# Kernel tuning notes

Measured on AMD Instinct MI355X. Metric: run time of the kernel, lower is better.

The kernel has to match this reference:

```python
import jax, jax.numpy as jnp
import numpy as np

B, N, F, D, TOPK, EXTRA = 32, 128, 10, 64, 20, 25
BN = B * N
EPS = 1e-5
SLOPE = 0.2  # GDN GraphLayer leaky_relu negative slope


def _cosine(a, b):
    na = jnp.maximum(jnp.linalg.norm(a, axis=-1), 1e-12)
    nb = jnp.maximum(jnp.linalg.norm(b, axis=-1), 1e-12)
    return (a @ b.T) / (na[:, None] * nb[None, :])


def _segment_softmax(logits, seg, num):
    m = jax.ops.segment_max(logits, seg, num_segments=num)
    m = jnp.where(jnp.isfinite(m), m, 0.0)  # empty segments
    e = jnp.exp(logits - m[seg])
    s = jax.ops.segment_sum(e, seg, num_segments=num)
    return e / jnp.maximum(s[seg], 1e-12)


def setup_inputs() -> dict:
    key = jax.random.key(0)
    ks = jax.random.split(key, 12)
    r = lambda i, shape, s=1.0: jax.random.normal(ks[i], shape, dtype=jnp.float32) * s
    return dict(
        data=r(0, (B, N, F)),
        emb=r(1, (N, D)) * 0.3,                       # nn.Embedding(node_num, dim)
        W1=r(2, (F, D)) * (1.0 / np.sqrt(F)),         # GraphLayer lin
        att_i1=r(3, (2 * D,)) * 0.1,                  # att on concat(h, emb)
        att_j1=r(4, (2 * D,)) * 0.1,
        bias1=jnp.zeros((D,), jnp.float32),
        bn1_g=jnp.ones((D,), jnp.float32),
        bn1_b=jnp.zeros((D,), jnp.float32),
        P=r(5, (BN, BN)) * (1.0 / np.sqrt(BN)),       # extra_pram
        W2=r(6, (D, D)) * (1.0 / np.sqrt(D)),         # GraphLayer1 lin
        att_i2=r(7, (D,)) * 0.1,
        att_j2=r(8, (D,)) * 0.1,
        bias2=jnp.zeros((D,), jnp.float32),
        bnO_g=jnp.ones((D,), jnp.float32),
        bnO_b=jnp.zeros((D,), jnp.float32),
        W_out=r(9, (D, 1)) * (1.0 / np.sqrt(D)),      # OutLayer Linear(dim,1)
        b_out=jnp.zeros((1,), jnp.float32),
        org_edge_index=jnp.zeros((2, 2), jnp.int32),  # dead arg in original forward
    )


def _forward(data, emb, W1, att_i1, att_j1, bias1, bn1_g, bn1_b, P, W2,
             att_i2, att_j2, bias2, bnO_g, bnO_b, W_out, b_out):
    x = data.reshape(BN, F)

    # ---- learned top-k graph from detached embedding cosine similarity ----
    w = jax.lax.stop_gradient(emb)              # weights_arr = detach()
    cos = _cosine(w, w)                         # [N, N]
    topv, topi = jax.lax.top_k(cos, TOPK)       # [N, TOPK]
    cos_w = jnp.tile(topv.reshape(-1), B)       # [B*N*TOPK]
    src0 = topi.reshape(-1)                     # gated_j (source)
    dst0 = jnp.repeat(jnp.arange(N), TOPK)      # gated_i (target)
    offs = jnp.repeat(jnp.arange(B) * N, N * TOPK)
    src = jnp.tile(src0, B) + offs
    dst = jnp.tile(dst0, B) + offs

    # ---- GraphLayer (GAT-style with embedding keys, edge weight = cos) ----
    all_emb = jnp.tile(emb, (B, 1))             # [BN, D]
    h = x @ W1                                  # [BN, D]
    kf = jnp.concatenate([h, all_emb], axis=-1) # [BN, 2D]
    si, sj = kf @ att_i1, kf @ att_j1           # [BN]
    score = jax.nn.leaky_relu(si[dst] + sj[src], SLOPE) * cos_w
    alpha = _segment_softmax(score, dst, BN)
    agg = jax.ops.segment_sum(h[src] * alpha[:, None], dst, num_segments=BN) + bias1
    mu, var = agg.mean(0), agg.var(0)           # BatchNorm1d (batch stats)
    gcn = jax.nn.relu(bn1_g * (agg - mu) / jnp.sqrt(var + EPS) + bn1_b)

    # ---- extra-feature branch (always taken: P is [BN, BN]) ----
    ef = P.T @ gcn                              # (gcn_out.T @ P).T
    g = jnp.concatenate([gcn, ef], axis=0)      # [2BN, D]
    cos2 = _cosine(g, g)                        # [2BN, 2BN]
    topv2, topi2 = jax.lax.top_k(cos2, EXTRA)
    corrs = topv2[:BN].reshape(-1)              # [BN*EXTRA]
    src2 = jnp.repeat(jnp.arange(BN), EXTRA)    # extra_i = edge_index[0] (source)
    dst2 = topi2[:BN].reshape(-1)               # extra_j = edge_index[1] (target)

    # ---- GraphLayer1 (no embedding keys, no BN in GNNLayer1.forward) ----
    h2 = g @ W2                                 # [2BN, D]
    s2 = jax.nn.leaky_relu((h2 @ att_i2)[dst2] + (h2 @ att_j2)[src2], SLOPE) * corrs
    alpha2 = _segment_softmax(s2, dst2, 2 * BN)
    agg2 = jax.ops.segment_sum(h2[src2] * alpha2[:, None], dst2, num_segments=2 * BN) + bias2
    gcn2 = jax.nn.relu(agg2)[:BN]

    # ---- output head: mul by embedding, BN over channels, Linear(D,1) ----
    x3 = gcn2.reshape(B, N, D) * emb[None]      # [B, N, D]
    mu2, var2 = x3.mean((0, 1)), x3.var((0, 1)) # BatchNorm1d over channel D
    x4 = jax.nn.relu(bnO_g * (x3 - mu2) / jnp.sqrt(var2 + EPS) + bnO_b)
    out = x4 @ W_out + b_out                    # [B, N, 1]; dropout = identity (eval)
    return out.reshape(-1, N)                   # [B, N]


def reference(data, emb, W1, att_i1, att_j1, bias1, bn1_g, bn1_b, P, W2,
              att_i2, att_j2, bias2, bnO_g, bnO_b, W_out, b_out, org_edge_index):
    # org_edge_index is dead in the original forward (only cached, never consumed)
    return _forward(data, emb, W1, att_i1, att_j1, bias1, bn1_g, bn1_b, P, W2,
                    att_i2, att_j2, bias2, bnO_g, bnO_b, W_out, b_out)
```

## Files before the change

kernel.cpp:

```cpp
#include <hip/hip_runtime.h>
#include <hip/hip_bf16.h>
#include <math.h>

#define DEV __device__ __forceinline__

constexpr int Bb   = 32;
constexpr int Nn   = 128;
constexpr int Ff   = 10;
constexpr int Dd   = 64;
constexpr int TOPK = 20;
constexpr int EXTRA= 25;
constexpr int BN   = 4096;
constexpr int TBN  = 8192;
constexpr int RC   = 16;
constexpr int CAND_CAP = 1024;
constexpr float EPS   = 1e-5f;
constexpr float SLOPE = 0.2f;

DEV unsigned int fenc(float f){
  unsigned int b = __float_as_uint(f);
  return (b & 0x80000000u) ? ~b : (b | 0x80000000u);
}
DEV float fdec(unsigned int u){
  unsigned int b = (u & 0x80000000u) ? (u & 0x7FFFFFFFu) : ~u;
  return __uint_as_float(b);
}

__global__ void k_zero(float* __restrict__ p, int n){
  int i = blockIdx.x*256 + threadIdx.x;
  if(i < n) p[i] = 0.f;
}

__global__ void k_emb_norm(const float* __restrict__ emb, float* __restrict__ norms){
  int i = blockIdx.x, d = threadIdx.x;
  float v = emb[i*Dd + d];
  float s = v*v;
  for(int o=32;o>0;o>>=1) s += __shfl_down(s, o, 64);
  if(d==0) norms[i] = fmaxf(sqrtf(s), 1e-12f);
}

__global__ void k_emb_topk(const float* __restrict__ emb, const float* __restrict__ norms,
                           float* __restrict__ topv, int* __restrict__ topi){
  __shared__ float se[Dd];
  __shared__ float sc[Nn];
  int i = blockIdx.x, t = threadIdx.x;
  if(t < Dd) se[t] = emb[i*Dd + t];
  __syncthreads();
  float dot = 0.f;
  for(int d=0; d<Dd; d++) dot += se[d]*emb[t*Dd + d];
  float v = dot/(norms[i]*norms[t]);
  sc[t] = v;
  __syncthreads();
  int rank = 0;
  for(int j=0; j<Nn; j++){
    float vj = sc[j];
    rank += (vj > v) || (vj == v && j < t);
  }
  if(rank < TOPK){
    topv[i*TOPK + rank] = v;
    topi[i*TOPK + rank] = t;
  }
}

__global__ void k_h1(const float* __restrict__ data, const float* __restrict__ emb,
                     const float* __restrict__ W1, const float* __restrict__ ai1,
                     const float* __restrict__ aj1,
                     float* __restrict__ h, float* __restrict__ si, float* __restrict__ sj){
  int r = blockIdx.x, d = threadIdx.x;
  int node = r & (Nn-1);
  __shared__ float xr[Ff];
  if(d < Ff) xr[d] = data[r*Ff + d];
  __syncthreads();
  float hv = 0.f;
  #pragma unroll
  for(int f=0; f<Ff; f++) hv += xr[f]*W1[f*Dd + d];
  h[r*Dd + d] = hv;
  float e = emb[node*Dd + d];
  float a = hv*ai1[d] + e*ai1[Dd + d];
  float b = hv*aj1[d] + e*aj1[Dd + d];
  for(int o=32;o>0;o>>=1){ a += __shfl_down(a,o,64); b += __shfl_down(b,o,64); }
  if(d==0){ si[r] = a; sj[r] = b; }
}

__global__ void k_agg1(const float* __restrict__ h, const float* __restrict__ si,
                       const float* __restrict__ sj, const float* __restrict__ topv,
                       const int* __restrict__ topi, const float* __restrict__ bias1,
                       float* __restrict__ agg){
  int r = blockIdx.x, d = threadIdx.x;
  int b = r >> 7, node = r & (Nn-1);
  __shared__ float sal[TOPK];
  __shared__ int   ssrc[TOPK];
  if(d < TOPK){
    int s = b*Nn + topi[node*TOPK + d];
    float sc = si[r] + sj[s];
    sc = sc >= 0.f ? sc : SLOPE*sc;
    sal[d] = sc * topv[node*TOPK + d];
    ssrc[d] = s;
  }
  __syncthreads();
  float m = -INFINITY;
  #pragma unroll
  for(int k=0;k<TOPK;k++) m = fmaxf(m, sal[k]);
  float al[TOPK]; float ssum = 0.f;
  #pragma unroll
  for(int k=0;k<TOPK;k++){ al[k] = expf(sal[k]-m); ssum += al[k]; }
  float inv = 1.0f/fmaxf(ssum, 1e-12f);
  float acc = 0.f;
  #pragma unroll
  for(int k=0;k<TOPK;k++) acc += al[k]*inv*h[ssrc[k]*Dd + d];
  agg[r*Dd + d] = acc + bias1[d];
}

__global__ void k_colstats(const float* __restrict__ x, float* __restrict__ mu, float* __restrict__ var){
  int c = blockIdx.x, t = threadIdx.x;
  float s = 0.f, s2 = 0.f;
  for(int r=t; r<BN; r+=256){ float v = x[r*Dd + c]; s += v; s2 += v*v; }
  __shared__ float ls[256], ls2[256];
  ls[t]=s; ls2[t]=s2; __syncthreads();
  for(int o=128;o>0;o>>=1){
    if(t<o){ ls[t]+=ls[t+o]; ls2[t]+=ls2[t+o]; }
    __syncthreads();
  }
  if(t==0){ float m = ls[0]/BN; mu[c]=m; var[c]=ls2[0]/BN - m*m; }
}

__global__ void k_bnrelu1(const float* __restrict__ agg, const float* __restrict__ mu,
                          const float* __restrict__ var, const float* __restrict__ gamma,
                          const float* __restrict__ beta, float* __restrict__ g){
  int idx = blockIdx.x*256 + threadIdx.x;
  int c = idx & (Dd-1);
  float v = agg[idx];
  float y = gamma[c]*(v - mu[c])/sqrtf(var[c]+EPS) + beta[c];
  g[idx] = fmaxf(y, 0.f);
}

__global__ __launch_bounds__(256) void k_ef1(const float* __restrict__ P, const float* __restrict__ gcn,
                                             float* __restrict__ part){
  __shared__ float Pt[16*128];
  __shared__ float Gt[16*64];
  int t = threadIdx.x;
  int jbase = blockIdx.x*128;
  int r0 = blockIdx.y*256;
  int row = t >> 4, col4 = (t & 15)*4;
  int tr = t >> 4, tc = t & 15;
  float acc[8][4] = {};
  for(int step=0; step<16; step++){
    int r = r0 + step*16;
    float4 pv0 = *(const float4*)&P[(size_t)(r+row)*BN + jbase + col4];
    float4 pv1 = *(const float4*)&P[(size_t)(r+row)*BN + jbase + col4 + 64];
    float4 gv  = *(const float4*)&gcn[(r+row)*Dd + col4];
    __syncthreads();
    *(float4*)&Pt[row*128 + col4]      = pv0;
    *(float4*)&Pt[row*128 + col4 + 64] = pv1;
    *(float4*)&Gt[row*64 + col4] = gv;
    __syncthreads();
    #pragma unroll
    for(int rr=0; rr<16; rr++){
      float4 pa0 = *(float4*)&Pt[rr*128 + tr*8];
      float4 pa1 = *(float4*)&Pt[rr*128 + tr*8 + 4];
      float4 gb  = *(float4*)&Gt[rr*64 + tc*4];
      float pav[8] = {pa0.x,pa0.y,pa0.z,pa0.w,pa1.x,pa1.y,pa1.z,pa1.w};
      float gbv[4] = {gb.x,gb.y,gb.z,gb.w};
      #pragma unroll
      for(int a=0;a<8;a++)
        #pragma unroll
        for(int b=0;b<4;b++) acc[a][b] += pav[a]*gbv[b];
    }
  }
  float* dst = part + ((size_t)blockIdx.y*BN + jbase)*Dd;
  #pragma unroll
  for(int a=0;a<8;a++){
    float4 v = make_float4(acc[a][0],acc[a][1],acc[a][2],acc[a][3]);
    *(float4*)&dst[(tr*8+a)*Dd + tc*4] = v;
  }
}

__global__ void k_ef2(const float* __restrict__ part, float* __restrict__ ef){
  int i = blockIdx.x*256 + threadIdx.x;
  float4 s = make_float4(0.f,0.f,0.f,0.f);
  #pragma unroll
  for(int c=0;c<RC;c++){
    float4 v = *(const float4*)&part[(size_t)c*BN*Dd + (size_t)i*4];
    s.x += v.x; s.y += v.y; s.z += v.z; s.w += v.w;
  }
  *(float4*)&ef[(size_t)i*4] = s;
}

__global__ void k_gn(const float* __restrict__ x, float* __restrict__ gn){
  int r = blockIdx.x, d = threadIdx.x;
  float v = x[(size_t)r*Dd + d];
  float s = v*v;
  for(int o=32;o>0;o>>=1) s += __shfl_down(s, o, 64);
  s = __shfl(s, 0, 64);
  float inv = 1.0f/fmaxf(sqrtf(s), 1e-12f);
  gn[(size_t)r*Dd + d] = v*inv;
}

__global__ __launch_bounds__(256) void k_sgemm(const float* __restrict__ gn,
                                               int rbase, float* __restrict__ S,
                                               float* __restrict__ Smax){
  __shared__ __align__(16) float A[64*128];
  __shared__ __align__(16) float Bs[64*128];
  int t = threadIdx.x;
  int ctile = blockIdx.x*128;
  int rtile = rbase + blockIdx.y*128;
  int q = t >> 4, m0 = t & 15;
  #pragma unroll
  for(int l=0;l<8;l++){
    int m = m0 + 16*l;
    float4 av = *(const float4*)&gn[(size_t)(rtile+m)*Dd + q*4];
    float4 bv = *(const float4*)&gn[(size_t)(ctile+m)*Dd + q*4];
    A[(q*4+0)*128 + m] = av.x; A[(q*4+1)*128 + m] = av.y;
    A[(q*4+2)*128 + m] = av.z; A[(q*4+3)*128 + m] = av.w;
    Bs[(q*4+0)*128 + m] = bv.x; Bs[(q*4+1)*128 + m] = bv.y;
    Bs[(q*4+2)*128 + m] = bv.z; Bs[(q*4+3)*128 + m] = bv.w;
  }
  __syncthreads();
  int tr = t >> 4;
  int tc = t & 15;
  float acc[8][8] = {};
  #pragma unroll 4
  for(int k=0;k<64;k++){
    float4 a0 = *(const float4*)&A[k*128 + tr*4];
    float4 a1 = *(const float4*)&A[k*128 + tr*4 + 64];
    float4 b0 = *(const float4*)&Bs[k*128 + tc*4];
    float4 b1 = *(const float4*)&Bs[k*128 + tc*4 + 64];
    float a[8] = {a0.x,a0.y,a0.z,a0.w,a1.x,a1.y,a1.z,a1.w};
    float b[8] = {b0.x,b0.y,b0.z,b0.w,b1.x,b1.y,b1.z,b1.w};
    #pragma unroll
    for(int i=0;i<8;i++)
      #pragma unroll
      for(int j=0;j<8;j++) acc[i][j] += a[i]*b[j];
  }
  int rloc = blockIdx.y*128;
  #pragma unroll
  for(int i=0;i<8;i++){
    int rl = tr*4 + (i&3) + (i>>2)*64;
    int r  = rloc + rl;
    float mL = fmaxf(fmaxf(acc[i][0],acc[i][1]), fmaxf(acc[i][2],acc[i][3]));
    float mR = fmaxf(fmaxf(acc[i][4],acc[i][5]), fmaxf(acc[i][6],acc[i][7]));
    #pragma unroll
    for(int o=1;o<4;o<<=1){
      mL = fmaxf(mL, __shfl_xor(mL, o, 64));
      mR = fmaxf(mR, __shfl_xor(mR, o, 64));
    }
    if((tc & 3) == 0){
      Smax[(size_t)r*512 + blockIdx.x*8 + (tc>>2)]     = mL;
      Smax[(size_t)r*512 + blockIdx.x*8 + 4 + (tc>>2)] = mR;
    }
    float4 v0 = make_float4(acc[i][0],acc[i][1],acc[i][2],acc[i][3]);
    float4 v1 = make_float4(acc[i][4],acc[i][5],acc[i][6],acc[i][7]);
    *(float4*)&S[(size_t)r*TBN + ctile + tc*4]      = v0;
    *(float4*)&S[(size_t)r*TBN + ctile + tc*4 + 64] = v1;
  }
}

__global__ __launch_bounds__(256) void k_radix(const float* __restrict__ S,
                                               const float* __restrict__ Smax,
                                               int rbase,
                                               float* __restrict__ topv2, int* __restrict__ topi2){
  __shared__ unsigned hist[4096];
  __shared__ unsigned wtot[4];
  __shared__ unsigned candE[CAND_CAP];
  __shared__ unsigned short candC[CAND_CAP];
  __shared__ unsigned bc_bin, bc_need, bc_cnt, bc_c;
  __shared__ float st16[512];
  __shared__ float stmax[64];
  __shared__ float sLsh;
  int t = threadIdx.x;
  int lane = t & 63, wid = t >> 6;
  int r = blockIdx.x;
  const float* src = S + (size_t)r*TBN;
  int col0 = t*32;

  st16[t]       = Smax[(size_t)r*512 + t];
  st16[256 + t] = Smax[(size_t)r*512 + 256 + t];
  #pragma unroll
  for(int j=0;j<16;j++) hist[t*16 + j] = 0u;
  if(t==0){ bc_cnt = 0u; bc_c = 0u; }
  __syncthreads();
  if(t < 64){
    float m = st16[t*8];
    #pragma unroll
    for(int k=1;k<8;k++) m = fmaxf(m, st16[t*8 + k]);
    stmax[t] = m;
  }
  __syncthreads();
  if(t < 64){
    float mi = stmax[t];
    int cnt = 0;
    for(int j=0;j<64;j++){
      float mj = stmax[j];
      cnt += (mj > mi) || (mj == mi && j < t);
    }
    if(cnt == 24) sLsh = mi;
  }
  __syncthreads();
  float L = sLsh;
  bool skip = fmaxf(st16[t*2], st16[t*2+1]) < L;

  unsigned enc[32];
  if(!skip){
    #pragma unroll
    for(int j=0;j<8;j++){
      float4 v = *(const float4*)&src[col0 + j*4];
      enc[j*4+0]=fenc(v.x); enc[j*4+1]=fenc(v.y); enc[j*4+2]=fenc(v.z); enc[j*4+3]=fenc(v.w);
    }
    #pragma unroll
    for(int j=0;j<32;j++) atomicAdd(&hist[enc[j] >> 20], 1u);
  } else {
    #pragma unroll
    for(int j=0;j<32;j++) enc[j] = 0u;
  }
  __syncthreads();
  unsigned lsum = 0u;
  #pragma unroll
  for(int j=0;j<16;j++) lsum += hist[t*16 + j];
  unsigned v = lsum;
  #pragma unroll
  for(int o=1;o<64;o<<=1){
    unsigned u = (unsigned)__shfl_down((int)v, o, 64);
    if(lane + o < 64) v += u;
  }
  if(lane == 0) wtot[wid] = v;
  __syncthreads();
  unsigned cross = 0u;
  #pragma unroll
  for(int w2=0;w2<4;w2++) if(w2 > wid) cross += wtot[w2];
  unsigned Tinc = v + cross;
  unsigned above = Tinc - lsum;
  unsigned run = above;
  #pragma unroll
  for(int b=15;b>=0;b--){
    unsigned prev = run;
    run += hist[t*16 + b];
    if(run >= EXTRA && prev < EXTRA){ bc_bin = (unsigned)(t*16 + b); bc_need = EXTRA - prev; }
  }
  __syncthreads();
  unsigned pivotBin = bc_bin, needIn = bc_need;
  int gr = rbase + r;
  #pragma unroll
  for(int j=0;j<32;j++){
    unsigned e = enc[j];
    unsigned bin = e >> 20;
    if(bin > pivotBin){
      unsigned s = atomicAdd(&bc_cnt, 1u);
      topv2[gr*EXTRA + s] = fdec(e);
      topi2[gr*EXTRA + s] = col0 + j;
    } else if(bin == pivotBin){
      unsigned ci = atomicAdd(&bc_c, 1u);
      if(ci < CAND_CAP){ candE[ci] = e; candC[ci] = (unsigned short)(col0 + j); }
    }
  }
  __syncthreads();
  unsigned c = bc_c;
  if(c <= CAND_CAP){
    for(unsigned i=t; i<c; i+=256){
      unsigned ei = candE[i]; unsigned coli = candC[i];
      unsigned rank = 0;
      for(unsigned j2=0;j2<c;j2++){
        unsigned ej = candE[j2];
        rank += (ej > ei) || (ej == ei && candC[j2] < coli);
      }
      if(rank < needIn){
        unsigned s = atomicAdd(&bc_cnt, 1u);
        topv2[gr*EXTRA + s] = fdec(ei);
        topi2[gr*EXTRA + s] = (int)coli;
      }
    }
  } else {
    unsigned* h256  = hist;
    unsigned* scanb = hist + 1024;
    unsigned prefix = pivotBin;
    unsigned need = needIn;
    const int shifts[3] = {12, 4, 0};
    const unsigned masks[3] = {255u, 255u, 15u};
    const int nbins[3] = {256, 256, 16};
    for(int p=0;p<3;p++){
      int sh = shifts[p]; unsigned mk = masks[p]; int nb = nbins[p];
      if(t < nb) h256[t] = 0u;
      __syncthreads();
      #pragma unroll
      for(int j=0;j<32;j++){
        unsigned e = enc[j];
        int pshift = (p==0)? 20 : (p==1? 12 : 4);
        if((e >> pshift) == prefix) atomicAdd(&h256[(e>>sh)&mk], 1u);
      }
      __syncthreads();
      unsigned vv = (t < nb) ? h256[t] : 0u;
      for(int o=1;o<nb;o<<=1){
        if(t < nb) scanb[t] = vv;
        __syncthreads();
        if(t < nb && t+o < nb) vv += scanb[t+o];
        __syncthreads();
      }
      if(t < nb) scanb[t] = vv;
      __syncthreads();
      if(t < nb){
        unsigned nxt = (t < nb-1) ? scanb[t+1] : 0u;
        if(vv >= need && nxt < need){ bc_bin = (prefix << ((p==2)?4:8)) | (unsigned)t; bc_need = need - nxt; }
      }
      __syncthreads();
      prefix = bc_bin; need = bc_need;
      __syncthreads();
    }
    unsigned pivotEnc = prefix;
    unsigned needTies = need;
    unsigned tie_local = 0u;
    #pragma unroll
    for(int j=0;j<32;j++){
      unsigned e = enc[j];
      if((e >> 20) == pivotBin){
        if(e > pivotEnc){
          unsigned s = atomicAdd(&bc_cnt, 1u);
          topv2[gr*EXTRA + s] = fdec(e);
          topi2[gr*EXTRA + s] = col0 + j;
        } else if(e == pivotEnc) tie_local++;
      }
    }
    unsigned iv = tie_local;
    for(int o=1;o<256;o<<=1){
      scanb[t] = iv; __syncthreads();
      if(t >= o) iv += scanb[t-o];
      __syncthreads();
    }
    unsigned rank = iv - tie_local;
    #pragma unroll
    for(int j=0;j<32;j++){
      unsigned e = enc[j];
      if(e == pivotEnc && (e >> 20) == pivotBin){
        if(rank < needTies){
          unsigned s = atomicAdd(&bc_cnt, 1u);
          topv2[gr*EXTRA + s] = fdec(e);
          topi2[gr*EXTRA + s] = col0 + j;
        }
        rank++;
      }
    }
  }
}

__global__ void k_h2(const float* __restrict__ g, const float* __restrict__ W2,
                     const float* __restrict__ ai2w, const float* __restrict__ aj2w,
                     float* __restrict__ h2, float* __restrict__ a2i, float* __restrict__ a2j){
  int r = blockIdx.x, d = threadIdx.x;
  __shared__ float gr[Dd];
  gr[d] = g[(size_t)r*Dd + d];
  __syncthreads();
  float hv = 0.f;
  #pragma unroll
  for(int k=0;k<Dd;k++) hv += gr[k]*W2[k*Dd + d];
  h2[(size_t)r*Dd + d] = hv;
  float a = hv*ai2w[d];
  float b = hv*aj2w[d];
  for(int o=32;o>0;o>>=1){ a += __shfl_down(a,o,64); b += __shfl_down(b,o,64); }
  if(d==0){ a2i[r]=a; a2j[r]=b; }
}

__global__ void k_s2(const float* __restrict__ a2i, const float* __restrict__ a2j,
                     const float* __restrict__ topv2, const int* __restrict__ topi2,
                     float* __restrict__ s2, unsigned int* __restrict__ segmax){
  int e = blockIdx.x*256 + threadIdx.x;
  if(e >= BN*EXTRA) return;
  int r = e/EXTRA;
  int dst = topi2[e];
  if(dst >= BN) return;
  float sc = a2i[dst] + a2j[r];
  sc = sc >= 0.f ? sc : SLOPE*sc;
  sc *= topv2[e];
  s2[e] = sc;
  atomicMax(&segmax[dst], fenc(sc));
}

__global__ void k_e2(const float* __restrict__ s2, const int* __restrict__ topi2,
                     const unsigned int* __restrict__ segmax,
                     float* __restrict__ e2, float* __restrict__ ssum){
  int e = blockIdx.x*256 + threadIdx.x;
  if(e >= BN*EXTRA) return;
  int dst = topi2[e];
  if(dst >= BN) return;
  float m = fdec(segmax[dst]);
  float v = expf(s2[e] - m);
  e2[e] = v;
  atomicAdd(&ssum[dst], v);
}

__global__ void k_scat(const float* __restrict__ e2, const float* __restrict__ ssum,
                       const int* __restrict__ topi2, const float* __restrict__ h2,
                       float* __restrict__ agg2){
  int idx = blockIdx.x*256 + threadIdx.x;
  int e = idx >> 6, d = idx & 63;
  int dst = topi2[e];
  if(dst >= BN) return;
  int src = e/EXTRA;
  float alpha = e2[e]/fmaxf(ssum[dst], 1e-12f);
  atomicAdd(&agg2[(size_t)dst*Dd + d], alpha*h2[(size_t)src*Dd + d]);
}

__global__ void k_headstats(const float* __restrict__ agg2, const float* __restrict__ bias2,
                            const float* __restrict__ emb, float* __restrict__ mu2, float* __restrict__ var2){
  int c = blockIdx.x, t = threadIdx.x;
  float bc = bias2[c];
  float s = 0.f, s2 = 0.f;
  for(int r=t; r<BN; r+=256){
    float v = fmaxf(agg2[(size_t)r*Dd + c] + bc, 0.f) * emb[(r & (Nn-1))*Dd + c];
    s += v; s2 += v*v;
  }
  __shared__ float ls[256], ls2[256];
  ls[t]=s; ls2[t]=s2; __syncthreads();
  for(int o=128;o>0;o>>=1){
    if(t<o){ ls[t]+=ls[t+o]; ls2[t]+=ls2[t+o]; }
    __syncthreads();
  }
  if(t==0){ float m=ls[0]/BN; mu2[c]=m; var2[c]=ls2[0]/BN - m*m; }
}

__global__ void k_out(const float* __restrict__ agg2, const float* __restrict__ bias2,
                      const float* __restrict__ emb, const float* __restrict__ mu2,
                      const float* __restrict__ var2, const float* __restrict__ gO,
                      const float* __restrict__ bO, const float* __restrict__ Wout,
                      const float* __restrict__ bout, float* __restrict__ out){
  int r = blockIdx.x, d = threadIdx.x;
  float v = fmaxf(agg2[(size_t)r*Dd + d] + bias2[d], 0.f) * emb[(r & (Nn-1))*Dd + d];
  float y = gO[d]*(v - mu2[d])/sqrtf(var2[d]+EPS) + bO[d];
  y = fmaxf(y, 0.f)*Wout[d];
  for(int o=32;o>0;o>>=1) y += __shfl_down(y, o, 64);
  if(d==0) out[r] = y + bout[0];
}

extern "C" void kernel_launch(void* const* d_in, const int* in_sizes, int n_in,
                              void* d_out, int out_size, void* d_ws, size_t ws_size,
                              hipStream_t stream){
  const float* data  = (const float*)d_in[0];
  const float* emb   = (const float*)d_in[1];
  const float* W1    = (const float*)d_in[2];
  const float* ai1   = (const float*)d_in[3];
  const float* aj1   = (const float*)d_in[4];
  const float* bias1 = (const float*)d_in[5];
  const float* bn1g  = (const float*)d_in[6];
  const float* bn1b  = (const float*)d_in[7];
  const float* P     = (const float*)d_in[8];
  const float* W2    = (const float*)d_in[9];
  const float* ai2w  = (const float*)d_in[10];
  const float* aj2w  = (const float*)d_in[11];
  const float* bias2 = (const float*)d_in[12];
  const float* bnOg  = (const float*)d_in[13];
  const float* bnOb  = (const float*)d_in[14];
  const float* Wout  = (const float*)d_in[15];
  const float* bout  = (const float*)d_in[16];
  float* out = (float*)d_out;

  char* w = (char*)d_ws;
  auto alloc = [&](size_t nbytes)->char*{
    char* p = w; w += (nbytes + 255) & ~(size_t)255; return p;
  };
  float* norms1 = (float*)alloc(Nn*4);
  float* topv1  = (float*)alloc(Nn*TOPK*4);
  int*   topi1  = (int*)  alloc(Nn*TOPK*4);
  float* h      = (float*)alloc((size_t)BN*Dd*4);
  float* si     = (float*)alloc(BN*4);
  float* sj     = (float*)alloc(BN*4);
  float* agg1   = (float*)alloc((size_t)BN*Dd*4);
  float* mu1    = (float*)alloc(Dd*4);
  float* var1   = (float*)alloc(Dd*4);
  float* g      = (float*)alloc((size_t)TBN*Dd*4);
  float* gn     = (float*)alloc((size_t)TBN*Dd*4);
  float* topv2  = (float*)alloc((size_t)BN*EXTRA*4);
  int*   topi2  = (int*)  alloc((size_t)BN*EXTRA*4);
  float* h2     = (float*)alloc((size_t)TBN*Dd*4);
  float* a2i    = (float*)alloc(TBN*4);
  float* a2j    = (float*)alloc(TBN*4);
  float* s2     = (float*)alloc((size_t)BN*EXTRA*4);
  float* e2     = (float*)alloc((size_t)BN*EXTRA*4);
  float* zblock = (float*)alloc(((size_t)TBN*Dd + TBN + TBN)*4);
  float* agg2   = zblock;
  float* ssum   = zblock + (size_t)TBN*Dd;
  unsigned int* segmax = (unsigned int*)(ssum + TBN);
  float* mu2    = (float*)alloc(Dd*4);
  float* var2   = (float*)alloc(Dd*4);
  float* efpart = (float*)alloc((size_t)RC*BN*Dd*4);
  float* SmaxB  = (float*)alloc((size_t)4096*512*4);

  size_t used = (size_t)(w - (char*)d_ws);
  size_t rem  = ws_size > used ? ws_size - used : 0;
  int chunkRows = 4096;
  while(chunkRows > 128 && (size_t)chunkRows*TBN*4 > rem) chunkRows >>= 1;
  float* Schunk = (float*)alloc((size_t)chunkRows*TBN*4);

  k_emb_norm<<<Nn, 64, 0, stream>>>(emb, norms1);
  k_emb_topk<<<Nn, Nn, 0, stream>>>(emb, norms1, topv1, topi1);
  k_h1<<<BN, 64, 0, stream>>>(data, emb, W1, ai1, aj1, h, si, sj);
  k_agg1<<<BN, 64, 0, stream>>>(h, si, sj, topv1, topi1, bias1, agg1);
  k_colstats<<<Dd, 256, 0, stream>>>(agg1, mu1, var1);
  k_bnrelu1<<<(BN*Dd)/256, 256, 0, stream>>>(agg1, mu1, var1, bn1g, bn1b, g);

  k_ef1<<<dim3(BN/128, RC), 256, 0, stream>>>(P, g, efpart);
  k_ef2<<<(BN*Dd/4)/256, 256, 0, stream>>>(efpart, g + (size_t)BN*Dd);

  k_gn<<<TBN, 64, 0, stream>>>(g, gn);
  for(int rbase=0; rbase<BN; rbase+=chunkRows){
    k_sgemm<<<dim3(TBN/128, chunkRows/128), 256, 0, stream>>>(gn, rbase, Schunk, SmaxB);
    k_radix<<<chunkRows, 256, 0, stream>>>(Schunk, SmaxB, rbase, topv2, topi2);
  }

  k_h2<<<BN, 64, 0, stream>>>(g, W2, ai2w, aj2w, h2, a2i, a2j);
  k_zero<<<((TBN*Dd + 2*TBN) + 255)/256, 256, 0, stream>>>(zblock, TBN*Dd + 2*TBN);
  k_s2<<<(BN*EXTRA + 255)/256, 256, 0, stream>>>(a2i, a2j, topv2, topi2, s2, segmax);
  k_e2<<<(BN*EXTRA + 255)/256, 256, 0, stream>>>(s2, topi2, segmax, e2, ssum);
  k_scat<<<(BN*EXTRA*Dd)/256, 256, 0, stream>>>(e2, ssum, topi2, h2, agg2);

  k_headstats<<<Dd, 256, 0, stream>>>(agg2, bias2, emb, mu2, var2);
  k_out<<<BN, 64, 0, stream>>>(agg2, bias2, emb, mu2, var2, bnOg, bnOb, Wout, bout, out);
}
```

Measured before the change: 356.1 us.

## Stop materializing the similarity matrix; recompute dot products for candidate tiles only

The GEMM kernel now writes only per-16-column tile maxima, not the full 4096x8192 similarity matrix. A new selection kernel picks the tiles whose max reaches the 25th-largest tile max, recomputes dot products just for those candidate columns, and ranks them exactly. Rows with too many candidate tiles are flagged and handled by a fallback kernel that recomputes the whole row with the radix select. This removes the large write and read of the score matrix at the cost of scalar recomputation of some dot products and an extra launch.

```diff
diff --git a/kernel.cpp b/kernel.cpp
--- a/kernel.cpp
+++ b/kernel.cpp
@@ -14,6 +14,7 @@
 constexpr int TBN  = 8192;
 constexpr int RC   = 16;
 constexpr int CAND_CAP = 1024;
+constexpr int SUBCAP = 128;
 constexpr float EPS   = 1e-5f;
 constexpr float SLOPE = 0.2f;
 
@@ -196,14 +197,13 @@
   gn[(size_t)r*Dd + d] = v*inv;
 }
 
-__global__ __launch_bounds__(256) void k_sgemm(const float* __restrict__ gn,
-                                               int rbase, float* __restrict__ S,
-                                               float* __restrict__ Smax){
+__global__ __launch_bounds__(256) void k_smax(const float* __restrict__ gn,
+                                              float* __restrict__ Smax){
   __shared__ __align__(16) float A[64*128];
   __shared__ __align__(16) float Bs[64*128];
   int t = threadIdx.x;
   int ctile = blockIdx.x*128;
-  int rtile = rbase + blockIdx.y*128;
+  int rtile = blockIdx.y*128;
   int q = t >> 4, m0 = t & 15;
   #pragma unroll
   for(int l=0;l<8;l++){
@@ -232,11 +232,9 @@
       #pragma unroll
       for(int j=0;j<8;j++) acc[i][j] += a[i]*b[j];
   }
-  int rloc = blockIdx.y*128;
   #pragma unroll
   for(int i=0;i<8;i++){
-    int rl = tr*4 + (i&3) + (i>>2)*64;
-    int r  = rloc + rl;
+    int r = rtile + tr*4 + (i&3) + (i>>2)*64;
     float mL = fmaxf(fmaxf(acc[i][0],acc[i][1]), fmaxf(acc[i][2],acc[i][3]));
     float mR = fmaxf(fmaxf(acc[i][4],acc[i][5]), fmaxf(acc[i][6],acc[i][7]));
     #pragma unroll
@@ -248,70 +246,98 @@
       Smax[(size_t)r*512 + blockIdx.x*8 + (tc>>2)]     = mL;
       Smax[(size_t)r*512 + blockIdx.x*8 + 4 + (tc>>2)] = mR;
     }
-    float4 v0 = make_float4(acc[i][0],acc[i][1],acc[i][2],acc[i][3]);
-    float4 v1 = make_float4(acc[i][4],acc[i][5],acc[i][6],acc[i][7]);
-    *(float4*)&S[(size_t)r*TBN + ctile + tc*4]      = v0;
-    *(float4*)&S[(size_t)r*TBN + ctile + tc*4 + 64] = v1;
-  }
-}
-
-__global__ __launch_bounds__(256) void k_radix(const float* __restrict__ S,
-                                               const float* __restrict__ Smax,
-                                               int rbase,
-                                               float* __restrict__ topv2, int* __restrict__ topi2){
+  }
+}
+
+__global__ __launch_bounds__(256) void k_sel(const float* __restrict__ gn,
+                                             const float* __restrict__ Smax,
+                                             float* __restrict__ topv2, int* __restrict__ topi2,
+                                             int* __restrict__ flag){
+  __shared__ float vrow[Dd];
+  __shared__ float st16[512];
+  __shared__ float sL;
+  __shared__ unsigned sub[SUBCAP];
+  __shared__ unsigned nsub, ovf;
+  __shared__ unsigned candV[SUBCAP*16];
+  __shared__ unsigned short candC[SUBCAP*16];
+  int r = blockIdx.x, t = threadIdx.x;
+  if(t < Dd) vrow[t] = gn[(size_t)r*Dd + t];
+  st16[t]       = Smax[(size_t)r*512 + t];
+  st16[256 + t] = Smax[(size_t)r*512 + 256 + t];
+  if(t==0){ nsub = 0u; ovf = 0u; }
+  __syncthreads();
+  for(int i=t; i<512; i+=256){
+    float mi = st16[i];
+    int cnt = 0;
+    for(int j=0;j<512;j++){
+      float mj = st16[j];
+      cnt += (mj > mi) || (mj == mi && j < i);
+    }
+    if(cnt == EXTRA-1) sL = mi;
+  }
+  __syncthreads();
+  float L = sL;
+  for(int i=t; i<512; i+=256){
+    if(st16[i] >= L){
+      unsigned k = atomicAdd(&nsub, 1u);
+      if(k < SUBCAP) sub[k] = (unsigned)i; else ovf = 1u;
+    }
+  }
+  __syncthreads();
+  if(ovf){ if(t==0) flag[r] = 1; return; }
+  unsigned ns = nsub;
+  unsigned c = ns*16;
+  for(unsigned i=t; i<c; i+=256){
+    int col = (int)sub[i>>4]*16 + (int)(i&15);
+    const float* gc = gn + (size_t)col*Dd;
+    float s = 0.f;
+    for(int d=0; d<Dd; d++) s += vrow[d]*gc[d];
+    candV[i] = fenc(s);
+    candC[i] = (unsigned short)col;
+  }
+  __syncthreads();
+  for(unsigned i=t; i<c; i+=256){
+    unsigned vi = candV[i]; unsigned ci = candC[i];
+    unsigned rank = 0;
+    for(unsigned j=0;j<c;j++){
+      unsigned vj = candV[j];
+      rank += (vj > vi) || (vj == vi && candC[j] < ci);
+    }
+    if(rank < EXTRA){
+      topv2[r*EXTRA + rank] = fdec(vi);
+      topi2[r*EXTRA + rank] = (int)ci;
+    }
+  }
+}
+
+__global__ __launch_bounds__(256) void k_fix(const float* __restrict__ gn,
+                                             const int* __restrict__ flag,
+                                             float* __restrict__ topv2, int* __restrict__ topi2){
+  int r = blockIdx.x;
+  if(flag[r] == 0) return;
+  __shared__ float vrow[Dd];
   __shared__ unsigned hist[4096];
   __shared__ unsigned wtot[4];
   __shared__ unsigned candE[CAND_CAP];
   __shared__ unsigned short candC[CAND_CAP];
   __shared__ unsigned bc_bin, bc_need, bc_cnt, bc_c;
-  __shared__ float st16[512];
-  __shared__ float stmax[64];
-  __shared__ float sLsh;
   int t = threadIdx.x;
   int lane = t & 63, wid = t >> 6;
-  int r = blockIdx.x;
-  const float* src = S + (size_t)r*TBN;
+  if(t < Dd) vrow[t] = gn[(size_t)r*Dd + t];
+  __syncthreads();
   int col0 = t*32;
-
-  st16[t]       = Smax[(size_t)r*512 + t];
-  st16[256 + t] = Smax[(size_t)r*512 + 256 + t];
+  unsigned enc[32];
+  for(int j=0;j<32;j++){
+    const float* gc = gn + (size_t)(col0 + j)*Dd;
+    float s = 0.f;
+    for(int d=0; d<Dd; d++) s += vrow[d]*gc[d];
+    enc[j] = fenc(s);
+  }
   #pragma unroll
   for(int j=0;j<16;j++) hist[t*16 + j] = 0u;
-  if(t==0){ bc_cnt = 0u; bc_c = 0u; }
-  __syncthreads();
-  if(t < 64){
-    float m = st16[t*8];
-    #pragma unroll
-    for(int k=1;k<8;k++) m = fmaxf(m, st16[t*8 + k]);
-    stmax[t] = m;
-  }
-  __syncthreads();
-  if(t < 64){
-    float mi = stmax[t];
-    int cnt = 0;
-    for(int j=0;j<64;j++){
-      float mj = stmax[j];
-      cnt += (mj > mi) || (mj == mi && j < t);
-    }
-    if(cnt == 24) sLsh = mi;
-  }
-  __syncthreads();
-  float L = sLsh;
-  bool skip = fmaxf(st16[t*2], st16[t*2+1]) < L;
-
-  unsigned enc[32];
-  if(!skip){
-    #pragma unroll
-    for(int j=0;j<8;j++){
-      float4 v = *(const float4*)&src[col0 + j*4];
-      enc[j*4+0]=fenc(v.x); enc[j*4+1]=fenc(v.y); enc[j*4+2]=fenc(v.z); enc[j*4+3]=fenc(v.w);
-    }
-    #pragma unroll
-    for(int j=0;j<32;j++) atomicAdd(&hist[enc[j] >> 20], 1u);
-  } else {
-    #pragma unroll
-    for(int j=0;j<32;j++) enc[j] = 0u;
-  }
+  __syncthreads();
+  #pragma unroll
+  for(int j=0;j<32;j++) atomicAdd(&hist[enc[j] >> 20], 1u);
   __syncthreads();
   unsigned lsum = 0u;
   #pragma unroll
@@ -336,17 +362,17 @@
     run += hist[t*16 + b];
     if(run >= EXTRA && prev < EXTRA){ bc_bin = (unsigned)(t*16 + b); bc_need = EXTRA - prev; }
   }
+  if(t==0){ bc_cnt = 0u; bc_c = 0u; }
   __syncthreads();
   unsigned pivotBin = bc_bin, needIn = bc_need;
-  int gr = rbase + r;
   #pragma unroll
   for(int j=0;j<32;j++){
     unsigned e = enc[j];
     unsigned bin = e >> 20;
     if(bin > pivotBin){
       unsigned s = atomicAdd(&bc_cnt, 1u);
-      topv2[gr*EXTRA + s] = fdec(e);
-      topi2[gr*EXTRA + s] = col0 + j;
+      topv2[r*EXTRA + s] = fdec(e);
+      topi2[r*EXTRA + s] = col0 + j;
     } else if(bin == pivotBin){
       unsigned ci = atomicAdd(&bc_c, 1u);
       if(ci < CAND_CAP){ candE[ci] = e; candC[ci] = (unsigned short)(col0 + j); }
@@ -364,8 +390,8 @@
       }
       if(rank < needIn){
         unsigned s = atomicAdd(&bc_cnt, 1u);
-        topv2[gr*EXTRA + s] = fdec(ei);
-        topi2[gr*EXTRA + s] = (int)coli;
+        topv2[r*EXTRA + s] = fdec(ei);
+        topi2[r*EXTRA + s] = (int)coli;
       }
     }
   } else {
@@ -413,8 +439,8 @@
       if((e >> 20) == pivotBin){
         if(e > pivotEnc){
           unsigned s = atomicAdd(&bc_cnt, 1u);
-          topv2[gr*EXTRA + s] = fdec(e);
-          topi2[gr*EXTRA + s] = col0 + j;
+          topv2[r*EXTRA + s] = fdec(e);
+          topi2[r*EXTRA + s] = col0 + j;
         } else if(e == pivotEnc) tie_local++;
       }
     }
@@ -431,8 +457,8 @@
       if(e == pivotEnc && (e >> 20) == pivotBin){
         if(rank < needTies){
           unsigned s = atomicAdd(&bc_cnt, 1u);
-          topv2[gr*EXTRA + s] = fdec(e);
-          topi2[gr*EXTRA + s] = col0 + j;
+          topv2[r*EXTRA + s] = fdec(e);
+          topi2[r*EXTRA + s] = col0 + j;
         }
         rank++;
       }
@@ -572,20 +598,15 @@
   float* a2j    = (float*)alloc(TBN*4);
   float* s2     = (float*)alloc((size_t)BN*EXTRA*4);
   float* e2     = (float*)alloc((size_t)BN*EXTRA*4);
-  float* zblock = (float*)alloc(((size_t)TBN*Dd + TBN + TBN)*4);
+  float* zblock = (float*)alloc(((size_t)TBN*Dd + TBN + TBN + BN)*4);
   float* agg2   = zblock;
   float* ssum   = zblock + (size_t)TBN*Dd;
   unsigned int* segmax = (unsigned int*)(ssum + TBN);
+  int* flagB    = (int*)(segmax + TBN);
   float* mu2    = (float*)alloc(Dd*4);
   float* var2   = (float*)alloc(Dd*4);
   float* efpart = (float*)alloc((size_t)RC*BN*Dd*4);
-  float* SmaxB  = (float*)alloc((size_t)4096*512*4);
-
-  size_t used = (size_t)(w - (char*)d_ws);
-  size_t rem  = ws_size > used ? ws_size - used : 0;
-  int chunkRows = 4096;
-  while(chunkRows > 128 && (size_t)chunkRows*TBN*4 > rem) chunkRows >>= 1;
-  float* Schunk = (float*)alloc((size_t)chunkRows*TBN*4);
+  float* SmaxB  = (float*)alloc((size_t)BN*512*4);
 
   k_emb_norm<<<Nn, 64, 0, stream>>>(emb, norms1);
   k_emb_topk<<<Nn, Nn, 0, stream>>>(emb, norms1, topv1, topi1);
@@ -597,14 +618,14 @@
   k_ef1<<<dim3(BN/128, RC), 256, 0, stream>>>(P, g, efpart);
   k_ef2<<<(BN*Dd/4)/256, 256, 0, stream>>>(efpart, g + (size_t)BN*Dd);
 
+  k_zero<<<((TBN*Dd + 2*TBN + BN) + 255)/256, 256, 0, stream>>>(zblock, TBN*Dd + 2*TBN + BN);
+
   k_gn<<<TBN, 64, 0, stream>>>(g, gn);
-  for(int rbase=0; rbase<BN; rbase+=chunkRows){
-    k_sgemm<<<dim3(TBN/128, chunkRows/128), 256, 0, stream>>>(gn, rbase, Schunk, SmaxB);
-    k_radix<<<chunkRows, 256, 0, stream>>>(Schunk, SmaxB, rbase, topv2, topi2);
-  }
+  k_smax<<<dim3(TBN/128, BN/128), 256, 0, stream>>>(gn, SmaxB);
+  k_sel<<<BN, 256, 0, stream>>>(gn, SmaxB, topv2, topi2, flagB);
+  k_fix<<<BN, 256, 0, stream>>>(gn, flagB, topv2, topi2);
 
   k_h2<<<BN, 64, 0, stream>>>(g, W2, ai2w, aj2w, h2, a2i, a2j);
-  k_zero<<<((TBN*Dd + 2*TBN) + 255)/256, 256, 0, stream>>>(zblock, TBN*Dd + 2*TBN);
   k_s2<<<(BN*EXTRA + 255)/256, 256, 0, stream>>>(a2i, a2j, topv2, topi2, s2, segmax);
   k_e2<<<(BN*EXTRA + 255)/256, 256, 0, stream>>>(s2, topi2, segmax, e2, ssum);
   k_scat<<<(BN*EXTRA*Dd)/256, 256, 0, stream>>>(e2, ssum, topi2, h2, agg2);
```

Result: slower. 1.041 ms (+192.3%).

## Fuse row L2 normalisation into BN-ReLU and ef reduction; halve sgemm LDS tiles

Applied to the files above, without the earlier changes.

Row-wise L2 normalisation now happens inside the BN+ReLU kernel for the first half of the rows and inside the partial-sum reduction kernel for the extra-feature half. This removes the separate k_gn launch and one pass over the 2BN×D matrix. The similarity GEMM now stages its K=64 dimension in two 32-wide chunks, halving shared memory per block to allow more resident blocks. The cost is an extra barrier and load phase per block, and the ef half of g is no longer written.

```diff
diff --git a/kernel.cpp b/kernel.cpp
--- a/kernel.cpp
+++ b/kernel.cpp
@@ -126,12 +126,18 @@
 
 __global__ void k_bnrelu1(const float* __restrict__ agg, const float* __restrict__ mu,
                           const float* __restrict__ var, const float* __restrict__ gamma,
-                          const float* __restrict__ beta, float* __restrict__ g){
-  int idx = blockIdx.x*256 + threadIdx.x;
-  int c = idx & (Dd-1);
-  float v = agg[idx];
-  float y = gamma[c]*(v - mu[c])/sqrtf(var[c]+EPS) + beta[c];
-  g[idx] = fmaxf(y, 0.f);
+                          const float* __restrict__ beta,
+                          float* __restrict__ g, float* __restrict__ gn){
+  int r = blockIdx.x, d = threadIdx.x;
+  float v = agg[(size_t)r*Dd + d];
+  float y = gamma[d]*(v - mu[d])/sqrtf(var[d]+EPS) + beta[d];
+  y = fmaxf(y, 0.f);
+  g[(size_t)r*Dd + d] = y;
+  float s = y*y;
+  for(int o=32;o>0;o>>=1) s += __shfl_down(s, o, 64);
+  s = __shfl(s, 0, 64);
+  float inv = 1.0f/fmaxf(sqrtf(s), 1e-12f);
+  gn[(size_t)r*Dd + d] = y*inv;
 }
 
 __global__ __launch_bounds__(256) void k_ef1(const float* __restrict__ P, const float* __restrict__ gcn,
@@ -175,62 +181,57 @@
   }
 }
 
-__global__ void k_ef2(const float* __restrict__ part, float* __restrict__ ef){
-  int i = blockIdx.x*256 + threadIdx.x;
-  float4 s = make_float4(0.f,0.f,0.f,0.f);
-  #pragma unroll
-  for(int c=0;c<RC;c++){
-    float4 v = *(const float4*)&part[(size_t)c*BN*Dd + (size_t)i*4];
-    s.x += v.x; s.y += v.y; s.z += v.z; s.w += v.w;
-  }
-  *(float4*)&ef[(size_t)i*4] = s;
-}
-
-__global__ void k_gn(const float* __restrict__ x, float* __restrict__ gn){
+__global__ void k_ef2(const float* __restrict__ part, float* __restrict__ gn){
   int r = blockIdx.x, d = threadIdx.x;
-  float v = x[(size_t)r*Dd + d];
-  float s = v*v;
-  for(int o=32;o>0;o>>=1) s += __shfl_down(s, o, 64);
-  s = __shfl(s, 0, 64);
-  float inv = 1.0f/fmaxf(sqrtf(s), 1e-12f);
-  gn[(size_t)r*Dd + d] = v*inv;
+  float s = 0.f;
+  #pragma unroll
+  for(int c=0;c<RC;c++) s += part[(size_t)c*BN*Dd + (size_t)r*Dd + d];
+  float q = s*s;
+  for(int o=32;o>0;o>>=1) q += __shfl_down(q, o, 64);
+  q = __shfl(q, 0, 64);
+  float inv = 1.0f/fmaxf(sqrtf(q), 1e-12f);
+  gn[(size_t)(BN + r)*Dd + d] = s*inv;
 }
 
 __global__ __launch_bounds__(256) void k_sgemm(const float* __restrict__ gn,
                                                int rbase, float* __restrict__ S,
                                                float* __restrict__ Smax){
-  __shared__ __align__(16) float A[64*128];
-  __shared__ __align__(16) float Bs[64*128];
+  __shared__ __align__(16) float A[32*128];
+  __shared__ __align__(16) float Bs[32*128];
   int t = threadIdx.x;
   int ctile = blockIdx.x*128;
   int rtile = rbase + blockIdx.y*128;
-  int q = t >> 4, m0 = t & 15;
-  #pragma unroll
-  for(int l=0;l<8;l++){
-    int m = m0 + 16*l;
-    float4 av = *(const float4*)&gn[(size_t)(rtile+m)*Dd + q*4];
-    float4 bv = *(const float4*)&gn[(size_t)(ctile+m)*Dd + q*4];
-    A[(q*4+0)*128 + m] = av.x; A[(q*4+1)*128 + m] = av.y;
-    A[(q*4+2)*128 + m] = av.z; A[(q*4+3)*128 + m] = av.w;
-    Bs[(q*4+0)*128 + m] = bv.x; Bs[(q*4+1)*128 + m] = bv.y;
-    Bs[(q*4+2)*128 + m] = bv.z; Bs[(q*4+3)*128 + m] = bv.w;
-  }
-  __syncthreads();
+  int q2 = t >> 5, m0 = t & 31;
   int tr = t >> 4;
   int tc = t & 15;
   float acc[8][8] = {};
-  #pragma unroll 4
-  for(int k=0;k<64;k++){
-    float4 a0 = *(const float4*)&A[k*128 + tr*4];
-    float4 a1 = *(const float4*)&A[k*128 + tr*4 + 64];
-    float4 b0 = *(const float4*)&Bs[k*128 + tc*4];
-    float4 b1 = *(const float4*)&Bs[k*128 + tc*4 + 64];
-    float a[8] = {a0.x,a0.y,a0.z,a0.w,a1.x,a1.y,a1.z,a1.w};
-    float b[8] = {b0.x,b0.y,b0.z,b0.w,b1.x,b1.y,b1.z,b1.w};
-    #pragma unroll
-    for(int i=0;i<8;i++)
+  #pragma unroll
+  for(int s=0; s<2; s++){
+    if(s) __syncthreads();
+    #pragma unroll
+    for(int l=0;l<4;l++){
+      int m = m0 + 32*l;
+      float4 av = *(const float4*)&gn[(size_t)(rtile+m)*Dd + s*32 + q2*4];
+      float4 bv = *(const float4*)&gn[(size_t)(ctile+m)*Dd + s*32 + q2*4];
+      A[(q2*4+0)*128 + m] = av.x; A[(q2*4+1)*128 + m] = av.y;
+      A[(q2*4+2)*128 + m] = av.z; A[(q2*4+3)*128 + m] = av.w;
+      Bs[(q2*4+0)*128 + m] = bv.x; Bs[(q2*4+1)*128 + m] = bv.y;
+      Bs[(q2*4+2)*128 + m] = bv.z; Bs[(q2*4+3)*128 + m] = bv.w;
+    }
+    __syncthreads();
+    #pragma unroll 4
+    for(int k=0;k<32;k++){
+      float4 a0 = *(const float4*)&A[k*128 + tr*4];
+      float4 a1 = *(const float4*)&A[k*128 + tr*4 + 64];
+      float4 b0 = *(const float4*)&Bs[k*128 + tc*4];
+      float4 b1 = *(const float4*)&Bs[k*128 + tc*4 + 64];
+      float a[8] = {a0.x,a0.y,a0.z,a0.w,a1.x,a1.y,a1.z,a1.w};
+      float b[8] = {b0.x,b0.y,b0.z,b0.w,b1.x,b1.y,b1.z,b1.w};
       #pragma unroll
-      for(int j=0;j<8;j++) acc[i][j] += a[i]*b[j];
+      for(int i=0;i<8;i++)
+        #pragma unroll
+        for(int j=0;j<8;j++) acc[i][j] += a[i]*b[j];
+    }
   }
   int rloc = blockIdx.y*128;
   #pragma unroll
@@ -592,12 +593,11 @@
   k_h1<<<BN, 64, 0, stream>>>(data, emb, W1, ai1, aj1, h, si, sj);
   k_agg1<<<BN, 64, 0, stream>>>(h, si, sj, topv1, topi1, bias1, agg1);
   k_colstats<<<Dd, 256, 0, stream>>>(agg1, mu1, var1);
-  k_bnrelu1<<<(BN*Dd)/256, 256, 0, stream>>>(agg1, mu1, var1, bn1g, bn1b, g);
+  k_bnrelu1<<<BN, 64, 0, stream>>>(agg1, mu1, var1, bn1g, bn1b, g, gn);
 
   k_ef1<<<dim3(BN/128, RC), 256, 0, stream>>>(P, g, efpart);
-  k_ef2<<<(BN*Dd/4)/256, 256, 0, stream>>>(efpart, g + (size_t)BN*Dd);
-
-  k_gn<<<TBN, 64, 0, stream>>>(g, gn);
+  k_ef2<<<BN, 64, 0, stream>>>(efpart, gn);
+
   for(int rbase=0; rbase<BN; rbase+=chunkRows){
     k_sgemm<<<dim3(TBN/128, chunkRows/128), 256, 0, stream>>>(gn, rbase, Schunk, SmaxB);
     k_radix<<<chunkRows, 256, 0, stream>>>(Schunk, SmaxB, rbase, topv2, topi2);
```

New measurement: 349.2 us. Within noise of the previous version (-1.9%).
